# Performance work log

Measured on AMD Instinct MI355X. Metric: run time of the kernel, lower is better.

Reference implementation:

```python
import jax, jax.numpy as jnp
import numpy as np

B, S, H, I, E, TOP_K = 2, 2048, 768, 3072, 7, 2


def setup_inputs() -> dict:
    key = jax.random.key(0)
    ks = jax.random.split(key, 5)
    x = jax.random.normal(ks[0], (B, S, H), dtype=jnp.float32)
    # parameter init ~ torch Linear default scale (1/sqrt(fan_in))
    wg = jax.random.normal(ks[1], (H, E), dtype=jnp.float32) / np.sqrt(H)
    bg = jnp.zeros((E,), dtype=jnp.float32)
    w1 = jax.random.normal(ks[2], (E, H, I), dtype=jnp.float32) / np.sqrt(H)
    b1 = jnp.zeros((E, I), dtype=jnp.float32)
    w2 = jax.random.normal(ks[3], (E, I, H), dtype=jnp.float32) / np.sqrt(I)
    b2 = jnp.zeros((E, H), dtype=jnp.float32)
    return {"x": x, "wg": wg, "bg": bg, "w1": w1, "b1": b1, "w2": w2, "b2": b2}


def _gate_weights(gate_logits):
    # top-k mask: -inf everywhere except top-k slots, then softmax.
    # Equivalent: softmax over top-k values, scattered back into [.., E].
    vals, idx = jax.lax.top_k(gate_logits, TOP_K)           # [B,S,K]
    wk = jax.nn.softmax(vals, axis=-1)                       # [B,S,K]
    onehot = jax.nn.one_hot(idx, E, dtype=gate_logits.dtype)  # [B,S,K,E]
    return jnp.einsum('bsk,bske->bse', wk, onehot)           # [B,S,E]


def reference(x, wg, bg, w1, b1, w2, b2):
    gate_logits = jnp.einsum('bsh,he->bse', x, wg) + bg      # [B,S,E]
    gate_w = _gate_weights(gate_logits)                       # [B,S,E]
    # dense all-expert FFN (the module evaluates EVERY expert on every token)
    h = jnp.einsum('bsh,ehi->bsei', x, w1) + b1              # [B,S,E,I]
    h = jax.nn.gelu(h, approximate=False)                    # torch.nn.GELU (exact erf)
    expert_out = jnp.einsum('bsei,eih->bseh', h, w2) + b2    # [B,S,E,H]
    out = jnp.einsum('bseh,bse->bsh', expert_out, gate_w)    # weighted combine
    # dropout is identity in eval mode
    return (out, gate_w)
```

## Files before the change

### kernel.cpp

```cpp
#include <hip/hip_runtime.h>
#include <hip/hip_bf16.h>
#include <cmath>

#define NT 4096
#define HD 768
#define ID 3072
#define NE 7
#define NP 8192
#define TM 256
#define TN 256
#define BK 32
#define KS 2
#define NT2 (HD / TN)
#define SLOTS 102
#define NRING 4
#define FFN1_MT 39
#define FFN1_NT (ID / TN)
#define FFN1_GRID (FFN1_NT * FFN1_MT)

using short8 = __attribute__((ext_vector_type(8))) short;
using f32x4  = __attribute__((ext_vector_type(4))) float;
typedef __hip_bfloat16 bf16;

typedef const __attribute__((address_space(1))) void* gas_ptr;
typedef __attribute__((address_space(3))) void* las_ptr;
#define GLDS(g, l) __builtin_amdgcn_global_load_lds((gas_ptr)(g), (las_ptr)(l), 16, 0, 0)

#define BAR()   asm volatile("s_barrier" ::: "memory")
#define WAITL() asm volatile("s_waitcnt lgkmcnt(0)" ::: "memory")
#define WV8()   asm volatile("s_waitcnt vmcnt(8)" ::: "memory")
#define WV4()   asm volatile("s_waitcnt vmcnt(4)" ::: "memory")
#define WV0()   asm volatile("s_waitcnt vmcnt(0)" ::: "memory")
#define SCHEDB() __builtin_amdgcn_sched_barrier(0)

__device__ inline float b2f(unsigned short u) {
  unsigned v = (unsigned)u << 16; float f; __builtin_memcpy(&f, &v, 4); return f;
}

__device__ inline float gelu_erf(float v) {
  float xa = fabsf(v) * 0.70710678118654752f;
  float t  = __builtin_amdgcn_rcpf(1.0f + 0.3275911f * xa);
  float p  = t * (0.254829592f + t * (-0.284496736f + t * (1.421413741f +
             t * (-1.453152027f + t * 1.061405429f))));
  float er = 1.0f - p * __expf(-xa * xa);
  er = (v < 0.0f) ? -er : er;
  return 0.5f * v * (1.0f + er);
}

__global__ __launch_bounds__(64) void gate_kernel(
    const float* __restrict__ x, const float* __restrict__ wg, const float* __restrict__ bg,
    float* __restrict__ gate_out, bf16* __restrict__ xb,
    float* __restrict__ pair_w, int* __restrict__ tokexp)
{
  int t = blockIdx.x;
  int lane = threadIdx.x;
  const float* xr = x + (size_t)t * HD;
  float acc[NE];
#pragma unroll
  for (int e = 0; e < NE; e++) acc[e] = 0.f;
#pragma unroll
  for (int j = 0; j < HD / 64; j++) {
    int h = lane + j * 64;
    float xv = xr[h];
    xb[(size_t)t * HD + h] = __float2bfloat16(xv);
    const float* wr = wg + (size_t)h * NE;
#pragma unroll
    for (int e = 0; e < NE; e++) acc[e] += xv * wr[e];
  }
#pragma unroll
  for (int e = 0; e < NE; e++) {
    float v = acc[e];
    for (int s = 32; s > 0; s >>= 1) v += __shfl_down(v, s, 64);
    acc[e] = v;
  }
  if (lane == 0) {
    float lg[NE];
#pragma unroll
    for (int e = 0; e < NE; e++) lg[e] = acc[e] + bg[e];
    int i0 = 0;
    for (int e = 1; e < NE; e++) if (lg[e] > lg[i0]) i0 = e;
    int i1 = -1;
    for (int e = 0; e < NE; e++) {
      if (e == i0) continue;
      if (i1 < 0 || lg[e] > lg[i1]) i1 = e;
    }
    float v0 = lg[i0], v1 = lg[i1];
    float e1 = expf(v1 - v0);
    float inv = 1.f / (1.f + e1);
    float w0 = inv, w1v = e1 * inv;
    float* go = gate_out + (size_t)t * NE;
#pragma unroll
    for (int e = 0; e < NE; e++) go[e] = 0.f;
    go[i0] = w0; go[i1] = w1v;
    pair_w[2 * t + 0] = w0;
    pair_w[2 * t + 1] = w1v;
    tokexp[2 * t + 0] = i0;
    tokexp[2 * t + 1] = i1;
  }
}

__global__ __launch_bounds__(256) void route_kernel(
    const int* __restrict__ tokexp, int* __restrict__ elist, int* __restrict__ counts)
{
  __shared__ int wcnt[4];
  int e = blockIdx.x;
  int tid = threadIdx.x, wv = tid >> 6, ln = tid & 63;
  int base = 0;
  for (int chunk = 0; chunk < NP; chunk += 256) {
    int p = chunk + tid;
    bool m = (tokexp[p] == e);
    unsigned long long bal = __ballot(m);
    if (ln == 0) wcnt[wv] = __popcll(bal);
    __syncthreads();
    int pre = 0;
#pragma unroll
    for (int w = 0; w < 4; w++) pre += (w < wv) ? wcnt[w] : 0;
    int rank = pre + __popcll(bal & ((1ull << ln) - 1ull));
    if (m) elist[e * NP + base + rank] = p;
    base += wcnt[0] + wcnt[1] + wcnt[2] + wcnt[3];
    __syncthreads();
  }
  if (tid == 0) counts[e] = base;
}

__global__ __launch_bounds__(256) void transpose_cvt_kernel(
    const float* __restrict__ src, bf16* __restrict__ dst, int K, int N)
{
  __shared__ float tile[64][65];
  int e = blockIdx.z;
  int n0 = blockIdx.x * 64;
  int k0 = blockIdx.y * 64;
  const float* s = src + (size_t)e * K * N;
  bf16* d = dst + (size_t)e * K * N;
  int t = threadIdx.x;
  {
    int kk = t >> 4;
    int nc = (t & 15) << 2;
#pragma unroll
    for (int r = 0; r < 4; r++) {
      int k = kk + r * 16;
      float4 v = *(const float4*)(s + (size_t)(k0 + k) * N + n0 + nc);
      tile[k][nc + 0] = v.x; tile[k][nc + 1] = v.y;
      tile[k][nc + 2] = v.z; tile[k][nc + 3] = v.w;
    }
  }
  __syncthreads();
  {
    int c = t & 15;
    int nbase = t >> 4;
#pragma unroll
    for (int r = 0; r < 4; r++) {
      int n = nbase + r * 16;
      bf16 tmp[4];
#pragma unroll
      for (int i = 0; i < 4; i++) tmp[i] = __float2bfloat16(tile[4 * c + i][n]);
      ushort4 u; __builtin_memcpy(&u, tmp, 8);
      *(ushort4*)(d + (size_t)(n0 + n) * K + k0 + 4 * c) = u;
    }
  }
}


__global__ __launch_bounds__(512, 2) void ffn1_kernel(
    const bf16* __restrict__ xb, const bf16* __restrict__ w1t, const float* __restrict__ b1,
    const int* __restrict__ counts, const int* __restrict__ elist, bf16* __restrict__ hbuf)
{
  __shared__ bf16 As[NRING][TM][4][8];
  __shared__ bf16 Bs[NRING][TN][4][8];
  __shared__ int plist[TM];

  int tid = threadIdx.x;
  int raw = blockIdx.x;
  int xcd = raw & 7, pos = raw >> 3;
  int v = (xcd < 4) ? xcd * 59 + pos : 236 + (xcd - 4) * 58 + pos;
  int by = v / FFN1_NT, bx = v % FFN1_NT;

  int e, base = 0, cnt = 0, acct = 0;
  bool found = false;
  for (e = 0; e < NE; e++) {
    cnt = counts[e];
    int tiles = (cnt + TM - 1) / TM;
    if (by < acct + tiles) { base = (by - acct) * TM; found = true; break; }
    acct += tiles;
  }
  if (!found) return;

  if (tid < TM) {
    int r = base + tid;
    plist[tid] = (r < cnt) ? elist[e * NP + r] : -1;
  }
  __syncthreads();

  const int n0 = bx * TN;
  const bf16* Bsrc = w1t + (size_t)e * ID * HD;

  int c0 = tid, c1 = tid + 512;
  int r0 = c0 >> 2, k0 = (c0 & 3) ^ ((r0 >> 1) & 3);
  int r1 = c1 >> 2, k1 = (c1 & 3) ^ ((r1 >> 1) & 3);
  int pr0 = plist[r0], pr1 = plist[r1];
  const bf16* a0 = xb + (size_t)((pr0 >= 0 ? pr0 : 0) >> 1) * HD + k0 * 8;
  const bf16* a1 = xb + (size_t)((pr1 >= 0 ? pr1 : 0) >> 1) * HD + k1 * 8;
  const bf16* b0 = Bsrc + (size_t)(n0 + r0) * HD + k0 * 8;
  const bf16* b1v = Bsrc + (size_t)(n0 + r1) * HD + k1 * 8;

#define STAGE_A(t_) do { bf16* d_ = (bf16*)As + (size_t)((t_) & 3) * TM * 32;    \
    GLDS(a0 + (size_t)(t_) * BK, d_ + c0 * 8);                                   \
    GLDS(a1 + (size_t)(t_) * BK, d_ + c1 * 8); } while (0)
#define STAGE_B(t_) do { bf16* d_ = (bf16*)Bs + (size_t)((t_) & 3) * TN * 32;    \
    GLDS(b0 + (size_t)(t_) * BK, d_ + c0 * 8);                                   \
    GLDS(b1v + (size_t)(t_) * BK, d_ + c1 * 8); } while (0)

  int wave = tid >> 6, lane = tid & 63;
  int wm = (wave >> 2) * 128, wn = (wave & 3) * 64;
  int lr = lane & 15, quad = lane >> 4;
  int ph = quad ^ ((lr >> 1) & 3);

  f32x4 acc[8][4] = {};
  const int NIT = HD / BK;

  STAGE_A(0); STAGE_B(0);
  STAGE_A(1); STAGE_B(1);
  STAGE_A(2); STAGE_B(2);
  WV8(); BAR();

  for (int t = 0; t < NIT; ++t) {
    int q = t & 3;
    short8 af[4], bfr[4], af2[4];
#pragma unroll
    for (int mi = 0; mi < 4; mi++) af[mi] = *(const short8*)&As[q][wm + mi * 16 + lr][ph][0];
#pragma unroll
    for (int nj = 0; nj < 4; nj++) bfr[nj] = *(const short8*)&Bs[q][wn + nj * 16 + lr][ph][0];
    BAR();
    WAITL(); SCHEDB();
    __builtin_amdgcn_s_setprio(1);
#pragma unroll
    for (int mi = 0; mi < 4; mi++)
#pragma unroll
      for (int nj = 0; nj < 4; nj++)
        acc[mi][nj] = __builtin_amdgcn_mfma_f32_16x16x32_bf16(bfr[nj], af[mi], acc[mi][nj], 0, 0, 0);
    __builtin_amdgcn_s_setprio(0);
    if (t + 3 < NIT) STAGE_A(t + 3);
#pragma unroll
    for (int mi = 0; mi < 4; mi++) af2[mi] = *(const short8*)&As[q][wm + 64 + mi * 16 + lr][ph][0];
    if (t + 3 < NIT) STAGE_B(t + 3);
    if (t + 3 < NIT) { WV8(); } else if (t + 2 < NIT) { WV4(); } else if (t + 1 < NIT) { WV0(); }
    BAR();
    WAITL(); SCHEDB();
    __builtin_amdgcn_s_setprio(1);
#pragma unroll
    for (int mi = 0; mi < 4; mi++)
#pragma unroll
      for (int nj = 0; nj < 4; nj++)
        acc[4 + mi][nj] = __builtin_amdgcn_mfma_f32_16x16x32_bf16(bfr[nj], af2[mi], acc[4 + mi][nj], 0, 0, 0);
    __builtin_amdgcn_s_setprio(0);
  }
#undef STAGE_A
#undef STAGE_B

  const float* b1e = b1 + (size_t)e * ID;
#pragma unroll
  for (int mi = 0; mi < 8; mi++) {
    int mrow = wm + mi * 16 + lr;
    int p = plist[mrow];
    if (p >= 0) {
      bf16* drow = hbuf + (size_t)p * ID;
#pragma unroll
      for (int nj = 0; nj < 4; nj++) {
        int colb = n0 + wn + nj * 16 + (quad << 2);
        float4 bs = *(const float4*)(b1e + colb);
        bf16 o[4];
        o[0] = __float2bfloat16(gelu_erf(acc[mi][nj][0] + bs.x));
        o[1] = __float2bfloat16(gelu_erf(acc[mi][nj][1] + bs.y));
        o[2] = __float2bfloat16(gelu_erf(acc[mi][nj][2] + bs.z));
        o[3] = __float2bfloat16(gelu_erf(acc[mi][nj][3] + bs.w));
        ushort4 u; __builtin_memcpy(&u, o, 8);
        *(ushort4*)(drow + colb) = u;
      }
    }
  }
}

__global__ __launch_bounds__(512, 2) void ffn2_kernel(
    const bf16* __restrict__ hbuf, const bf16* __restrict__ w2t, const float* __restrict__ b2,
    const int* __restrict__ counts, const int* __restrict__ elist,
    const float* __restrict__ pair_w, bf16* __restrict__ pout)
{
  __shared__ bf16 As[NRING][TM][4][8];
  __shared__ bf16 Bs[NRING][TN][4][8];
  __shared__ int plist[TM];

  int tid = threadIdx.x;
  int xcd = blockIdx.x;
  int slot = blockIdx.y;
  int e = 0, seg = 0, base = 0, cnt = 0, n0 = 0;
  bool found = false;
  for (int p = xcd; p < 2 * NE; p += 8) {
    int pe = p >> 1;
    int c = counts[pe];
    int tiles = ((c + TM - 1) / TM) * NT2;
    if (slot < tiles) {
      e = pe; seg = p & 1; cnt = c;
      base = (slot / NT2) * TM;
      n0 = (slot % NT2) * TN;
      found = true; break;
    }
    slot -= tiles;
  }
  if (!found) return;

  if (tid < TM) {
    int r = base + tid;
    plist[tid] = (r < cnt) ? elist[e * NP + r] : -1;
  }
  __syncthreads();

  const int kbase = seg * (ID / KS);
  const bf16* Bsrc = w2t + (size_t)e * HD * ID;

  int c0 = tid, c1 = tid + 512;
  int r0 = c0 >> 2, k0 = (c0 & 3) ^ ((r0 >> 1) & 3);
  int r1 = c1 >> 2, k1 = (c1 & 3) ^ ((r1 >> 1) & 3);
  int pr0 = plist[r0], pr1 = plist[r1];
  const bf16* a0 = hbuf + (size_t)(pr0 >= 0 ? pr0 : 0) * ID + kbase + k0 * 8;
  const bf16* a1 = hbuf + (size_t)(pr1 >= 0 ? pr1 : 0) * ID + kbase + k1 * 8;
  const bf16* b0 = Bsrc + (size_t)(n0 + r0) * ID + kbase + k0 * 8;
  const bf16* b1v = Bsrc + (size_t)(n0 + r1) * ID + kbase + k1 * 8;

#define STAGE_A(t_) do { bf16* d_ = (bf16*)As + (size_t)((t_) & 3) * TM * 32;    \
    GLDS(a0 + (size_t)(t_) * BK, d_ + c0 * 8);                                   \
    GLDS(a1 + (size_t)(t_) * BK, d_ + c1 * 8); } while (0)
#define STAGE_B(t_) do { bf16* d_ = (bf16*)Bs + (size_t)((t_) & 3) * TN * 32;    \
    GLDS(b0 + (size_t)(t_) * BK, d_ + c0 * 8);                                   \
    GLDS(b1v + (size_t)(t_) * BK, d_ + c1 * 8); } while (0)

  int wave = tid >> 6, lane = tid & 63;
  int wm = (wave >> 2) * 128, wn = (wave & 3) * 64;
  int lr = lane & 15, quad = lane >> 4;
  int ph = quad ^ ((lr >> 1) & 3);

  f32x4 acc[8][4] = {};
  const int NIT = (ID / KS) / BK;

  STAGE_A(0); STAGE_B(0);
  STAGE_A(1); STAGE_B(1);
  STAGE_A(2); STAGE_B(2);
  WV8(); BAR();

  for (int t = 0; t < NIT; ++t) {
    int q = t & 3;
    short8 af[4], bfr[4], af2[4];
#pragma unroll
    for (int mi = 0; mi < 4; mi++) af[mi] = *(const short8*)&As[q][wm + mi * 16 + lr][ph][0];
#pragma unroll
    for (int nj = 0; nj < 4; nj++) bfr[nj] = *(const short8*)&Bs[q][wn + nj * 16 + lr][ph][0];
    BAR();
    WAITL(); SCHEDB();
    __builtin_amdgcn_s_setprio(1);
#pragma unroll
    for (int mi = 0; mi < 4; mi++)
#pragma unroll
      for (int nj = 0; nj < 4; nj++)
        acc[mi][nj] = __builtin_amdgcn_mfma_f32_16x16x32_bf16(bfr[nj], af[mi], acc[mi][nj], 0, 0, 0);
    __builtin_amdgcn_s_setprio(0);
    if (t + 3 < NIT) STAGE_A(t + 3);
#pragma unroll
    for (int mi = 0; mi < 4; mi++) af2[mi] = *(const short8*)&As[q][wm + 64 + mi * 16 + lr][ph][0];
    if (t + 3 < NIT) STAGE_B(t + 3);
    if (t + 3 < NIT) { WV8(); } else if (t + 2 < NIT) { WV4(); } else if (t + 1 < NIT) { WV0(); }
    BAR();
    WAITL(); SCHEDB();
    __builtin_amdgcn_s_setprio(1);
#pragma unroll
    for (int mi = 0; mi < 4; mi++)
#pragma unroll
      for (int nj = 0; nj < 4; nj++)
        acc[4 + mi][nj] = __builtin_amdgcn_mfma_f32_16x16x32_bf16(bfr[nj], af2[mi], acc[4 + mi][nj], 0, 0, 0);
    __builtin_amdgcn_s_setprio(0);
  }
#undef STAGE_A
#undef STAGE_B

  const float* b2e = b2 + (size_t)e * HD;
#pragma unroll
  for (int mi = 0; mi < 8; mi++) {
    int mrow = wm + mi * 16 + lr;
    int p = plist[mrow];
    if (p >= 0) {
      float pw = pair_w[p];
      bf16* drow = pout + ((size_t)seg * NP + p) * HD;
#pragma unroll
      for (int nj = 0; nj < 4; nj++) {
        int colb = n0 + wn + nj * 16 + (quad << 2);
        float bx_ = 0.f, by_ = 0.f, bz_ = 0.f, bw_ = 0.f;
        if (seg == 0) {
          float4 bs = *(const float4*)(b2e + colb);
          bx_ = bs.x; by_ = bs.y; bz_ = bs.z; bw_ = bs.w;
        }
        bf16 o[4];
        o[0] = __float2bfloat16((acc[mi][nj][0] + bx_) * pw);
        o[1] = __float2bfloat16((acc[mi][nj][1] + by_) * pw);
        o[2] = __float2bfloat16((acc[mi][nj][2] + bz_) * pw);
        o[3] = __float2bfloat16((acc[mi][nj][3] + bw_) * pw);
        ushort4 u; __builtin_memcpy(&u, o, 8);
        *(ushort4*)(drow + colb) = u;
      }
    }
  }
}

__global__ __launch_bounds__(192) void combine_kernel(
    const bf16* __restrict__ pout, float* __restrict__ out)
{
  int t = blockIdx.x, j = threadIdx.x;
  f32x4 o = {0.f, 0.f, 0.f, 0.f};
#pragma unroll
  for (int s = 0; s < KS; s++) {
#pragma unroll
    for (int k = 0; k < 2; k++) {
      const ushort4* v = (const ushort4*)(pout + ((size_t)s * NP + 2 * t + k) * HD);
      ushort4 u = v[j];
      o[0] += b2f(u.x); o[1] += b2f(u.y); o[2] += b2f(u.z); o[3] += b2f(u.w);
    }
  }
  ((f32x4*)(out + (size_t)t * HD))[j] = o;
}

extern "C" void kernel_launch(void* const* d_in, const int* in_sizes, int n_in,
                              void* d_out, int out_size, void* d_ws, size_t ws_size,
                              hipStream_t stream)
{
  const float* x  = (const float*)d_in[0];
  const float* wg = (const float*)d_in[1];
  const float* bg = (const float*)d_in[2];
  const float* w1 = (const float*)d_in[3];
  const float* b1 = (const float*)d_in[4];
  const float* w2 = (const float*)d_in[5];
  const float* b2 = (const float*)d_in[6];
  float* out = (float*)d_out;
  float* gate_out = out + (size_t)NT * HD;

  char* ws = (char*)d_ws;
  size_t off = 0;
  int* counts  = (int*)(ws + off);  off += 256;
  int* tokexp  = (int*)(ws + off);  off += (size_t)NP * 4;
  int* elist   = (int*)(ws + off);  off += (size_t)NE * NP * 4;
  float* pair_w = (float*)(ws + off); off += (size_t)NP * 4;
  bf16* xb   = (bf16*)(ws + off);   off += (size_t)NT * HD * 2;
  bf16* w1t  = (bf16*)(ws + off);   off += (size_t)NE * HD * ID * 2;
  bf16* w2t  = (bf16*)(ws + off);   off += (size_t)NE * HD * ID * 2;
  bf16* hbuf = (bf16*)(ws + off);   off += (size_t)NP * ID * 2;
  bf16* pout = (bf16*)(ws + off);   off += (size_t)KS * NP * HD * 2;

  gate_kernel<<<NT, 64, 0, stream>>>(x, wg, bg, gate_out, xb, pair_w, tokexp);
  route_kernel<<<NE, 256, 0, stream>>>(tokexp, elist, counts);
  transpose_cvt_kernel<<<dim3(ID / 64, HD / 64, NE), 256, 0, stream>>>(w1, w1t, HD, ID);
  transpose_cvt_kernel<<<dim3(HD / 64, ID / 64, NE), 256, 0, stream>>>(w2, w2t, ID, HD);
  ffn1_kernel<<<FFN1_GRID, 512, 0, stream>>>(xb, w1t, b1, counts, elist, hbuf);
  ffn2_kernel<<<dim3(8, SLOTS), 512, 0, stream>>>(hbuf, w2t, b2, counts, elist, pair_w, pout);
  combine_kernel<<<NT, 192, 0, stream>>>(pout, out);
}
```

Baseline: 337.9 us.

## Pre-gather routed tokens into contiguous per-expert buffer for FFN GEMMs

Adds a gather kernel that copies each expert's routed token rows into a contiguous compacted bf16 buffer, reusing the pout workspace. FFN1 and FFN2 then read A rows with plain strided addressing, and the hidden buffer is stored in compacted order. This removes the per-block plist build and its barrier from FFN1 and the first barrier in FFN2, and it makes A-tile loads contiguous instead of scattered. The cost is an extra kernel launch plus an extra read and write of the activations, and hbuf is padded so partial tiles can read past the end.

```diff
diff --git a/kernel.cpp b/kernel.cpp
--- a/kernel.cpp
+++ b/kernel.cpp
@@ -123,6 +123,30 @@
   if (tid == 0) counts[e] = base;
 }
 
+__global__ __launch_bounds__(256) void gather_kernel(
+    const bf16* __restrict__ xb, const int* __restrict__ elist,
+    const int* __restrict__ counts, bf16* __restrict__ xg)
+{
+  int e = blockIdx.x;
+  int m = blockIdx.y;
+  int cnt = counts[e];
+  int r0 = m * 16;
+  if (r0 >= cnt) return;
+  int ebase = 0;
+  for (int i = 0; i < e; i++) ebase += counts[i];
+  int tid = threadIdx.x;
+#pragma unroll
+  for (int i = 0; i < 6; i++) {
+    int seg = tid + i * 256;
+    int r = r0 + (seg / 96), o = (seg % 96) * 8;
+    if (r < cnt) {
+      int tok = elist[e * NP + r] >> 1;
+      *(uint4*)(xg + (size_t)(ebase + r) * HD + o) =
+        *(const uint4*)(xb + (size_t)tok * HD + o);
+    }
+  }
+}
+
 __global__ __launch_bounds__(256) void transpose_cvt_kernel(
     const float* __restrict__ src, bf16* __restrict__ dst, int K, int N)
 {
@@ -162,12 +186,11 @@
 
 
 __global__ __launch_bounds__(512, 2) void ffn1_kernel(
-    const bf16* __restrict__ xb, const bf16* __restrict__ w1t, const float* __restrict__ b1,
-    const int* __restrict__ counts, const int* __restrict__ elist, bf16* __restrict__ hbuf)
+    const bf16* __restrict__ xg, const bf16* __restrict__ w1t, const float* __restrict__ b1,
+    const int* __restrict__ counts, bf16* __restrict__ hbuf)
 {
   __shared__ bf16 As[NRING][TM][4][8];
   __shared__ bf16 Bs[NRING][TN][4][8];
-  __shared__ int plist[TM];
 
   int tid = threadIdx.x;
   int raw = blockIdx.x;
@@ -175,31 +198,25 @@
   int v = (xcd < 4) ? xcd * 59 + pos : 236 + (xcd - 4) * 58 + pos;
   int by = v / FFN1_NT, bx = v % FFN1_NT;
 
-  int e, base = 0, cnt = 0, acct = 0;
+  int e, base = 0, cnt = 0, acct = 0, ebase = 0;
   bool found = false;
   for (e = 0; e < NE; e++) {
     cnt = counts[e];
     int tiles = (cnt + TM - 1) / TM;
     if (by < acct + tiles) { base = (by - acct) * TM; found = true; break; }
-    acct += tiles;
+    acct += tiles; ebase += cnt;
   }
   if (!found) return;
 
-  if (tid < TM) {
-    int r = base + tid;
-    plist[tid] = (r < cnt) ? elist[e * NP + r] : -1;
-  }
-  __syncthreads();
-
   const int n0 = bx * TN;
+  const bf16* Asrc = xg + (size_t)(ebase + base) * HD;
   const bf16* Bsrc = w1t + (size_t)e * ID * HD;
 
   int c0 = tid, c1 = tid + 512;
   int r0 = c0 >> 2, k0 = (c0 & 3) ^ ((r0 >> 1) & 3);
   int r1 = c1 >> 2, k1 = (c1 & 3) ^ ((r1 >> 1) & 3);
-  int pr0 = plist[r0], pr1 = plist[r1];
-  const bf16* a0 = xb + (size_t)((pr0 >= 0 ? pr0 : 0) >> 1) * HD + k0 * 8;
-  const bf16* a1 = xb + (size_t)((pr1 >= 0 ? pr1 : 0) >> 1) * HD + k1 * 8;
+  const bf16* a0 = Asrc + (size_t)r0 * HD + k0 * 8;
+  const bf16* a1 = Asrc + (size_t)r1 * HD + k1 * 8;
   const bf16* b0 = Bsrc + (size_t)(n0 + r0) * HD + k0 * 8;
   const bf16* b1v = Bsrc + (size_t)(n0 + r1) * HD + k1 * 8;
 
@@ -261,9 +278,8 @@
 #pragma unroll
   for (int mi = 0; mi < 8; mi++) {
     int mrow = wm + mi * 16 + lr;
-    int p = plist[mrow];
-    if (p >= 0) {
-      bf16* drow = hbuf + (size_t)p * ID;
+    if (base + mrow < cnt) {
+      bf16* drow = hbuf + (size_t)(ebase + base + mrow) * ID;
 #pragma unroll
       for (int nj = 0; nj < 4; nj++) {
         int colb = n0 + wn + nj * 16 + (quad << 2);
@@ -292,7 +308,7 @@
   int tid = threadIdx.x;
   int xcd = blockIdx.x;
   int slot = blockIdx.y;
-  int e = 0, seg = 0, base = 0, cnt = 0, n0 = 0;
+  int e = 0, seg = 0, base = 0, cnt = 0, n0 = 0, ebase = 0;
   bool found = false;
   for (int p = xcd; p < 2 * NE; p += 8) {
     int pe = p >> 1;
@@ -302,27 +318,23 @@
       e = pe; seg = p & 1; cnt = c;
       base = (slot / NT2) * TM;
       n0 = (slot % NT2) * TN;
+      ebase = 0;
+      for (int i = 0; i < pe; i++) ebase += counts[i];
       found = true; break;
     }
     slot -= tiles;
   }
   if (!found) return;
 
-  if (tid < TM) {
-    int r = base + tid;
-    plist[tid] = (r < cnt) ? elist[e * NP + r] : -1;
-  }
-  __syncthreads();
-
   const int kbase = seg * (ID / KS);
+  const bf16* Asrc = hbuf + (size_t)(ebase + base) * ID + kbase;
   const bf16* Bsrc = w2t + (size_t)e * HD * ID;
 
   int c0 = tid, c1 = tid + 512;
   int r0 = c0 >> 2, k0 = (c0 & 3) ^ ((r0 >> 1) & 3);
   int r1 = c1 >> 2, k1 = (c1 & 3) ^ ((r1 >> 1) & 3);
-  int pr0 = plist[r0], pr1 = plist[r1];
-  const bf16* a0 = hbuf + (size_t)(pr0 >= 0 ? pr0 : 0) * ID + kbase + k0 * 8;
-  const bf16* a1 = hbuf + (size_t)(pr1 >= 0 ? pr1 : 0) * ID + kbase + k1 * 8;
+  const bf16* a0 = Asrc + (size_t)r0 * ID + k0 * 8;
+  const bf16* a1 = Asrc + (size_t)r1 * ID + k1 * 8;
   const bf16* b0 = Bsrc + (size_t)(n0 + r0) * ID + kbase + k0 * 8;
   const bf16* b1v = Bsrc + (size_t)(n0 + r1) * ID + kbase + k1 * 8;
 
@@ -344,6 +356,10 @@
   STAGE_A(0); STAGE_B(0);
   STAGE_A(1); STAGE_B(1);
   STAGE_A(2); STAGE_B(2);
+  if (tid < TM) {
+    int r = base + tid;
+    plist[tid] = (r < cnt) ? elist[e * NP + r] : -1;
+  }
   WV8(); BAR();
 
   for (int t = 0; t < NIT; ++t) {
@@ -448,14 +464,16 @@
   bf16* xb   = (bf16*)(ws + off);   off += (size_t)NT * HD * 2;
   bf16* w1t  = (bf16*)(ws + off);   off += (size_t)NE * HD * ID * 2;
   bf16* w2t  = (bf16*)(ws + off);   off += (size_t)NE * HD * ID * 2;
-  bf16* hbuf = (bf16*)(ws + off);   off += (size_t)NP * ID * 2;
+  bf16* hbuf = (bf16*)(ws + off);   off += (size_t)(NP + 256) * ID * 2;
   bf16* pout = (bf16*)(ws + off);   off += (size_t)KS * NP * HD * 2;
+  bf16* xg = pout;
 
   gate_kernel<<<NT, 64, 0, stream>>>(x, wg, bg, gate_out, xb, pair_w, tokexp);
   route_kernel<<<NE, 256, 0, stream>>>(tokexp, elist, counts);
+  gather_kernel<<<dim3(NE, 512), 256, 0, stream>>>(xb, elist, counts, xg);
   transpose_cvt_kernel<<<dim3(ID / 64, HD / 64, NE), 256, 0, stream>>>(w1, w1t, HD, ID);
   transpose_cvt_kernel<<<dim3(HD / 64, ID / 64, NE), 256, 0, stream>>>(w2, w2t, ID, HD);
-  ffn1_kernel<<<FFN1_GRID, 512, 0, stream>>>(xb, w1t, b1, counts, elist, hbuf);
+  ffn1_kernel<<<FFN1_GRID, 512, 0, stream>>>(xg, w1t, b1, counts, hbuf);
   ffn2_kernel<<<dim3(8, SLOTS), 512, 0, stream>>>(hbuf, w2t, b2, counts, elist, pair_w, pout);
   combine_kernel<<<NT, 192, 0, stream>>>(pout, out);
 }
```

Result: slower. 351.6 us (+4.1%).
